# Performance work log

Hardware: AMD Instinct MI355X
Metric: run time of the kernel (lower is better)

## Reference

```python
import jax, jax.numpy as jnp
import numpy as np

# per-class illumination constants (19 Cityscapes classes), pre-divided by 255
_NIGHT = jnp.asarray(np.array([76.5113984140019, 76.23163212875781, 60.90662084364415, 69.06930071129905, 69.63671393061327, 73.11413822794262, 140.7827781957324, 116.29554873008291, 46.23329954488532, 57.839322341112386, 32.61465346757989, 57.4385179294615, 62.234896087294814, 90.90285758569436, 91.99610158117673, 91.82209397173472, 94.06478985576457, 74.6924145472464, 69.15034088822232], dtype=np.float32) / 255.0)
_CITY = jnp.asarray(np.array([86.46051320057052, 79.37014543897092, 95.30679177391578, 71.11888521745776, 75.57026559270716, 77.90493757655786, 74.77466800282637, 88.27701037425895, 57.685269557270146, 72.71472387765841, 229.9589238353863, 66.9194012998903, 60.42471796718752, 76.8407421534007, 74.98657626719087, 73.56771430328095, 123.92515568872523, 68.93476495876828, 76.0970460111028], dtype=np.float32) / 255.0)

LOSS_WEIGHT = 1.0
GAMMA = 0.4


def setup_inputs() -> dict:
    key = jax.random.key(0)
    k1, k2, k3 = jax.random.split(key, 3)
    B, H, W = 8, 512, 1024
    reflectance = jax.random.uniform(k1, (B, 3, H, W), dtype=jnp.float32)
    org_img = jax.random.uniform(k2, (B, 3, H, W), dtype=jnp.float32)
    seg_label = jax.random.randint(k3, (B, 1, H, W), 0, 19, dtype=jnp.int64)
    return {"reflectance": reflectance, "org_img": org_img, "seg_label": seg_label}


def reference(reflectance, org_img, seg_label):
    # illumination = channel-wise max: [B,1,H,W]
    illum = jnp.max(org_img, axis=1, keepdims=True)
    # the 19-way masked subtract loop is a per-pixel table gather
    illum = illum - _NIGHT[seg_label]
    # min-max normalize over the whole tensor
    imin, imax = illum.min(), illum.max()
    illum = (illum - imin) / (imax - imin)
    # gamma correction (faithful to gamma(): divide by max, pow, re-scale)
    gmax = illum.max()
    illum = jnp.power(illum / gmax, GAMMA) * gmax
    # 19-way masked add loop == gather of cityscape table
    illum = jnp.clip(illum + _CITY[seg_label], 0.0, 1.0)
    bright = reflectance * illum  # broadcast [B,3,H,W] * [B,1,H,W]
    mean = jnp.mean(bright, axis=(0, 2, 3))  # [3] per-channel means
    r, g, b = mean[0], mean[1], mean[2]
    loss = LOSS_WEIGHT * ((r - g) ** 2 + (r - b) ** 2 + (g - b) ** 2)
    return loss
```

## Files before the change

### kernel.cpp

```cpp
#include <hip/hip_runtime.h>

#define HW_C   524288
#define NPIX   4194304
#define NG     (NPIX / 4)
#define GRID   1024
#define BLK    256
#define SLICE  (GRID * BLK)

__device__ __forceinline__ float fast_pow04(float x) {
    return __builtin_amdgcn_exp2f(0.4f * __builtin_amdgcn_logf(x));
}

__constant__ float c_night[19] = {
    (float)(76.5113984140019/255.0),  (float)(76.23163212875781/255.0),
    (float)(60.90662084364415/255.0), (float)(69.06930071129905/255.0),
    (float)(69.63671393061327/255.0), (float)(73.11413822794262/255.0),
    (float)(140.7827781957324/255.0), (float)(116.29554873008291/255.0),
    (float)(46.23329954488532/255.0), (float)(57.839322341112386/255.0),
    (float)(32.61465346757989/255.0), (float)(57.4385179294615/255.0),
    (float)(62.234896087294814/255.0),(float)(90.90285758569436/255.0),
    (float)(91.99610158117673/255.0), (float)(91.82209397173472/255.0),
    (float)(94.06478985576457/255.0), (float)(74.6924145472464/255.0),
    (float)(69.15034088822232/255.0)
};
__constant__ float c_city[19] = {
    (float)(86.46051320057052/255.0), (float)(79.37014543897092/255.0),
    (float)(95.30679177391578/255.0), (float)(71.11888521745776/255.0),
    (float)(75.57026559270716/255.0), (float)(77.90493757655786/255.0),
    (float)(74.77466800282637/255.0), (float)(88.27701037425895/255.0),
    (float)(57.685269557270146/255.0),(float)(72.71472387765841/255.0),
    (float)(229.9589238353863/255.0), (float)(66.9194012998903/255.0),
    (float)(60.42471796718752/255.0), (float)(76.8407421534007/255.0),
    (float)(74.98657626719087/255.0), (float)(73.56771430328095/255.0),
    (float)(123.92515568872523/255.0),(float)(68.93476495876828/255.0),
    (float)(76.0970460111028/255.0)
};

template<bool STORE>
__global__ __launch_bounds__(BLK, 4) void k_pass1(const float* __restrict__ org,
                                                  const int* __restrict__ seg,
                                                  float* __restrict__ illum,
                                                  uchar4* __restrict__ seg8,
                                                  float2* __restrict__ bmm)
{
    const int lane = threadIdx.x & 63;
    const float night_reg = c_night[lane < 19 ? lane : 0];
    const int t = blockIdx.x * BLK + threadIdx.x;

    float4 R[4], G[4], Bc[4];
    int4   S[4];
    int    P[4];

    #pragma unroll
    for (int k = 0; k < 4; ++k) {
        const int p = (t + k * SLICE) << 2;
        P[k] = p;
        const size_t base = (size_t)(p >> 19) * (3 * HW_C) + (p & (HW_C - 1));
        R[k]  = *(const float4*)(org + base);
        G[k]  = *(const float4*)(org + base + HW_C);
        Bc[k] = *(const float4*)(org + base + 2 * HW_C);
        S[k]  = *(const int4*)(seg + p);
    }

    float lmin = 1e30f, lmax = -1e30f;
    #pragma unroll
    for (int k = 0; k < 4; ++k) {
        float4 il;
        il.x = fmaxf(fmaxf(R[k].x, G[k].x), Bc[k].x) - __shfl(night_reg, S[k].x);
        il.y = fmaxf(fmaxf(R[k].y, G[k].y), Bc[k].y) - __shfl(night_reg, S[k].y);
        il.z = fmaxf(fmaxf(R[k].z, G[k].z), Bc[k].z) - __shfl(night_reg, S[k].z);
        il.w = fmaxf(fmaxf(R[k].w, G[k].w), Bc[k].w) - __shfl(night_reg, S[k].w);
        if (STORE) {
            *(float4*)(illum + P[k]) = il;
            seg8[P[k] >> 2] = make_uchar4((unsigned char)S[k].x, (unsigned char)S[k].y,
                                          (unsigned char)S[k].z, (unsigned char)S[k].w);
        }
        lmin = fminf(lmin, fminf(fminf(il.x, il.y), fminf(il.z, il.w)));
        lmax = fmaxf(lmax, fmaxf(fmaxf(il.x, il.y), fmaxf(il.z, il.w)));
    }

    #pragma unroll
    for (int m = 1; m < 64; m <<= 1) {
        lmin = fminf(lmin, __shfl_xor(lmin, m));
        lmax = fmaxf(lmax, __shfl_xor(lmax, m));
    }
    __shared__ float smin[BLK / 64], smax[BLK / 64];
    const int wave = threadIdx.x >> 6;
    if ((threadIdx.x & 63) == 0) { smin[wave] = lmin; smax[wave] = lmax; }
    __syncthreads();
    if (threadIdx.x == 0) {
        float m = smin[0], M = smax[0];
        #pragma unroll
        for (int w = 1; w < BLK / 64; ++w) { m = fminf(m, smin[w]); M = fmaxf(M, smax[w]); }
        bmm[blockIdx.x] = make_float2(m, M);
    }
}

template<bool STORE>
__global__ __launch_bounds__(BLK, 4) void k_pass2(const float* __restrict__ refl,
                                                  const float* __restrict__ org,
                                                  const int* __restrict__ seg,
                                                  const float* __restrict__ illum,
                                                  const uchar4* __restrict__ seg8,
                                                  const float2* __restrict__ bmm,
                                                  double* __restrict__ partial)
{
    const int lane = threadIdx.x & 63;
    const float city_reg  = c_city[lane < 19 ? lane : 0];
    const float night_reg = c_night[lane < 19 ? lane : 0];
    const int t = blockIdx.x * BLK + threadIdx.x;

    float2 mm[16];
    #pragma unroll
    for (int k = 0; k < 16; ++k) mm[k] = bmm[lane + k * 64];

    int P[4];
    size_t baseA[4];
    #pragma unroll
    for (int k = 0; k < 4; ++k) {
        const int p = (t + k * SLICE) << 2;
        P[k] = p;
        baseA[k] = (size_t)(p >> 19) * (3 * HW_C) + (p & (HW_C - 1));
    }

    float4 il[4]; uchar4 q[4];
    float4 oR[4], oG[4], oB[4]; int4 sv[4];
    if (STORE) {
        #pragma unroll
        for (int k = 0; k < 4; ++k) {
            il[k] = *(const float4*)(illum + P[k]);
            q[k]  = seg8[P[k] >> 2];
        }
    } else {
        #pragma unroll
        for (int k = 0; k < 4; ++k) {
            oR[k] = *(const float4*)(org + baseA[k]);
            oG[k] = *(const float4*)(org + baseA[k] + HW_C);
            oB[k] = *(const float4*)(org + baseA[k] + 2 * HW_C);
            sv[k] = *(const int4*)(seg + P[k]);
        }
    }
    float4 rr[4], gg[4], bb[4];
    #pragma unroll
    for (int k = 0; k < 4; ++k) {
        rr[k] = *(const float4*)(refl + baseA[k]);
        gg[k] = *(const float4*)(refl + baseA[k] + HW_C);
        bb[k] = *(const float4*)(refl + baseA[k] + 2 * HW_C);
    }

    float lmin = mm[0].x, lmax = mm[0].y;
    #pragma unroll
    for (int k = 1; k < 16; ++k) { lmin = fminf(lmin, mm[k].x); lmax = fmaxf(lmax, mm[k].y); }
    #pragma unroll
    for (int m = 1; m < 64; m <<= 1) {
        lmin = fminf(lmin, __shfl_xor(lmin, m));
        lmax = fmaxf(lmax, __shfl_xor(lmax, m));
    }
    const float imin = lmin;
    const float inv  = 1.0f / (lmax - lmin);

    float sr = 0.f, sg = 0.f, sb = 0.f;
    #pragma unroll
    for (int k = 0; k < 4; ++k) {
        float c0, c1, c2, c3;
        if (STORE) {
            c0 = __shfl(city_reg, (int)q[k].x); c1 = __shfl(city_reg, (int)q[k].y);
            c2 = __shfl(city_reg, (int)q[k].z); c3 = __shfl(city_reg, (int)q[k].w);
        } else {
            il[k].x = fmaxf(fmaxf(oR[k].x, oG[k].x), oB[k].x) - __shfl(night_reg, sv[k].x);
            il[k].y = fmaxf(fmaxf(oR[k].y, oG[k].y), oB[k].y) - __shfl(night_reg, sv[k].y);
            il[k].z = fmaxf(fmaxf(oR[k].z, oG[k].z), oB[k].z) - __shfl(night_reg, sv[k].z);
            il[k].w = fmaxf(fmaxf(oR[k].w, oG[k].w), oB[k].w) - __shfl(night_reg, sv[k].w);
            c0 = __shfl(city_reg, sv[k].x); c1 = __shfl(city_reg, sv[k].y);
            c2 = __shfl(city_reg, sv[k].z); c3 = __shfl(city_reg, sv[k].w);
        }
        float x, z;
        x = (il[k].x - imin) * inv; z = fminf(fmaxf(fast_pow04(x) + c0, 0.f), 1.f);
        sr += rr[k].x * z; sg += gg[k].x * z; sb += bb[k].x * z;
        x = (il[k].y - imin) * inv; z = fminf(fmaxf(fast_pow04(x) + c1, 0.f), 1.f);
        sr += rr[k].y * z; sg += gg[k].y * z; sb += bb[k].y * z;
        x = (il[k].z - imin) * inv; z = fminf(fmaxf(fast_pow04(x) + c2, 0.f), 1.f);
        sr += rr[k].z * z; sg += gg[k].z * z; sb += bb[k].z * z;
        x = (il[k].w - imin) * inv; z = fminf(fmaxf(fast_pow04(x) + c3, 0.f), 1.f);
        sr += rr[k].w * z; sg += gg[k].w * z; sb += bb[k].w * z;
    }

    double vr = sr, vg = sg, vb = sb;
    for (int off = 32; off > 0; off >>= 1) {
        vr += __shfl_down(vr, off);
        vg += __shfl_down(vg, off);
        vb += __shfl_down(vb, off);
    }
    __shared__ double sh[3][BLK / 64];
    const int wave = threadIdx.x >> 6;
    if ((threadIdx.x & 63) == 0) { sh[0][wave] = vr; sh[1][wave] = vg; sh[2][wave] = vb; }
    __syncthreads();
    if (threadIdx.x == 0) {
        double tr = 0, tg = 0, tb = 0;
        #pragma unroll
        for (int w = 0; w < BLK / 64; ++w) { tr += sh[0][w]; tg += sh[1][w]; tb += sh[2][w]; }
        partial[3 * blockIdx.x + 0] = tr;
        partial[3 * blockIdx.x + 1] = tg;
        partial[3 * blockIdx.x + 2] = tb;
    }
}

__global__ __launch_bounds__(BLK) void k_final(const double* __restrict__ partial,
                                               float* __restrict__ out)
{
    double sr = 0, sg = 0, sb = 0;
    for (int i = threadIdx.x; i < GRID; i += BLK) {
        sr += partial[3 * i + 0];
        sg += partial[3 * i + 1];
        sb += partial[3 * i + 2];
    }
    for (int off = 32; off > 0; off >>= 1) {
        sr += __shfl_down(sr, off);
        sg += __shfl_down(sg, off);
        sb += __shfl_down(sb, off);
    }
    __shared__ double sh[3][BLK / 64];
    const int wave = threadIdx.x >> 6;
    if ((threadIdx.x & 63) == 0) { sh[0][wave] = sr; sh[1][wave] = sg; sh[2][wave] = sb; }
    __syncthreads();
    if (threadIdx.x == 0) {
        double tr = 0, tg = 0, tb = 0;
        #pragma unroll
        for (int w = 0; w < BLK / 64; ++w) { tr += sh[0][w]; tg += sh[1][w]; tb += sh[2][w]; }
        const double n = (double)NPIX;
        const double r = tr / n, g = tg / n, b = tb / n;
        out[0] = (float)((r - g) * (r - g) + (r - b) * (r - b) + (g - b) * (g - b));
    }
}

extern "C" void kernel_launch(void* const* d_in, const int* in_sizes, int n_in,
                              void* d_out, int out_size, void* d_ws, size_t ws_size,
                              hipStream_t stream) {
    const float* refl = (const float*)d_in[0];
    const float* org  = (const float*)d_in[1];
    const int*   seg  = (const int*)d_in[2];
    float* out = (float*)d_out;

    unsigned char* wsb = (unsigned char*)d_ws;
    float2*  bmm     = (float2*)(wsb + 4096);
    double*  partial = (double*)(wsb + 24576);
    float*   illum   = (float*)(wsb + 131072);
    uchar4*  seg8    = (uchar4*)(wsb + 131072 + sizeof(float) * (size_t)NPIX);
    const size_t needed = 131072 + 5ull * (size_t)NPIX;
    const bool store = (ws_size >= needed);

    if (store) {
        k_pass1<true ><<<GRID, BLK, 0, stream>>>(org, seg, illum, seg8, bmm);
        k_pass2<true ><<<GRID, BLK, 0, stream>>>(refl, org, seg, illum, seg8, bmm, partial);
    } else {
        k_pass1<false><<<GRID, BLK, 0, stream>>>(org, seg, illum, seg8, bmm);
        k_pass2<false><<<GRID, BLK, 0, stream>>>(refl, org, seg, illum, seg8, bmm, partial);
    }
    k_final<<<1, BLK, 0, stream>>>(partial, out);
}
```

Measured before the change: 138.0 us.

## Recompute illumination in second pass instead of materializing it to workspace

Removes the path that wrote per-pixel illumination and packed labels to workspace in the first pass and read them back in the second. The second pass now always re-reads org_img and seg_label and recomputes channel max minus the night table. This relies on those inputs still being resident in the large last-level cache from the first pass, and saves roughly 20 MB of writes. It also reads the block min/max array as float4, and moves the reflectance loads into the accumulation loop to lower register pressure. The trade-off is more raw read traffic if the re-reads miss the cache.

```diff
diff --git a/kernel.cpp b/kernel.cpp
--- a/kernel.cpp
+++ b/kernel.cpp
@@ -36,11 +36,8 @@
     (float)(76.0970460111028/255.0)
 };
 
-template<bool STORE>
 __global__ __launch_bounds__(BLK, 4) void k_pass1(const float* __restrict__ org,
                                                   const int* __restrict__ seg,
-                                                  float* __restrict__ illum,
-                                                  uchar4* __restrict__ seg8,
                                                   float2* __restrict__ bmm)
 {
     const int lane = threadIdx.x & 63;
@@ -49,12 +46,10 @@
 
     float4 R[4], G[4], Bc[4];
     int4   S[4];
-    int    P[4];
 
     #pragma unroll
     for (int k = 0; k < 4; ++k) {
         const int p = (t + k * SLICE) << 2;
-        P[k] = p;
         const size_t base = (size_t)(p >> 19) * (3 * HW_C) + (p & (HW_C - 1));
         R[k]  = *(const float4*)(org + base);
         G[k]  = *(const float4*)(org + base + HW_C);
@@ -70,11 +65,6 @@
         il.y = fmaxf(fmaxf(R[k].y, G[k].y), Bc[k].y) - __shfl(night_reg, S[k].y);
         il.z = fmaxf(fmaxf(R[k].z, G[k].z), Bc[k].z) - __shfl(night_reg, S[k].z);
         il.w = fmaxf(fmaxf(R[k].w, G[k].w), Bc[k].w) - __shfl(night_reg, S[k].w);
-        if (STORE) {
-            *(float4*)(illum + P[k]) = il;
-            seg8[P[k] >> 2] = make_uchar4((unsigned char)S[k].x, (unsigned char)S[k].y,
-                                          (unsigned char)S[k].z, (unsigned char)S[k].w);
-        }
         lmin = fminf(lmin, fminf(fminf(il.x, il.y), fminf(il.z, il.w)));
         lmax = fmaxf(lmax, fmaxf(fmaxf(il.x, il.y), fmaxf(il.z, il.w)));
     }
@@ -96,12 +86,9 @@
     }
 }
 
-template<bool STORE>
 __global__ __launch_bounds__(BLK, 4) void k_pass2(const float* __restrict__ refl,
                                                   const float* __restrict__ org,
                                                   const int* __restrict__ seg,
-                                                  const float* __restrict__ illum,
-                                                  const uchar4* __restrict__ seg8,
                                                   const float2* __restrict__ bmm,
                                                   double* __restrict__ partial)
 {
@@ -110,9 +97,10 @@
     const float night_reg = c_night[lane < 19 ? lane : 0];
     const int t = blockIdx.x * BLK + threadIdx.x;
 
-    float2 mm[16];
-    #pragma unroll
-    for (int k = 0; k < 16; ++k) mm[k] = bmm[lane + k * 64];
+    const float4* bmm4 = (const float4*)bmm;
+    float4 mm[8];
+    #pragma unroll
+    for (int k = 0; k < 8; ++k) mm[k] = bmm4[lane + k * 64];
 
     int P[4];
     size_t baseA[4];
@@ -123,34 +111,21 @@
         baseA[k] = (size_t)(p >> 19) * (3 * HW_C) + (p & (HW_C - 1));
     }
 
-    float4 il[4]; uchar4 q[4];
     float4 oR[4], oG[4], oB[4]; int4 sv[4];
-    if (STORE) {
-        #pragma unroll
-        for (int k = 0; k < 4; ++k) {
-            il[k] = *(const float4*)(illum + P[k]);
-            q[k]  = seg8[P[k] >> 2];
-        }
-    } else {
-        #pragma unroll
-        for (int k = 0; k < 4; ++k) {
-            oR[k] = *(const float4*)(org + baseA[k]);
-            oG[k] = *(const float4*)(org + baseA[k] + HW_C);
-            oB[k] = *(const float4*)(org + baseA[k] + 2 * HW_C);
-            sv[k] = *(const int4*)(seg + P[k]);
-        }
-    }
-    float4 rr[4], gg[4], bb[4];
-    #pragma unroll
-    for (int k = 0; k < 4; ++k) {
-        rr[k] = *(const float4*)(refl + baseA[k]);
-        gg[k] = *(const float4*)(refl + baseA[k] + HW_C);
-        bb[k] = *(const float4*)(refl + baseA[k] + 2 * HW_C);
-    }
-
-    float lmin = mm[0].x, lmax = mm[0].y;
-    #pragma unroll
-    for (int k = 1; k < 16; ++k) { lmin = fminf(lmin, mm[k].x); lmax = fmaxf(lmax, mm[k].y); }
+    #pragma unroll
+    for (int k = 0; k < 4; ++k) {
+        oR[k] = *(const float4*)(org + baseA[k]);
+        oG[k] = *(const float4*)(org + baseA[k] + HW_C);
+        oB[k] = *(const float4*)(org + baseA[k] + 2 * HW_C);
+        sv[k] = *(const int4*)(seg + P[k]);
+    }
+
+    float lmin = fminf(mm[0].x, mm[0].z), lmax = fmaxf(mm[0].y, mm[0].w);
+    #pragma unroll
+    for (int k = 1; k < 8; ++k) {
+        lmin = fminf(lmin, fminf(mm[k].x, mm[k].z));
+        lmax = fmaxf(lmax, fmaxf(mm[k].y, mm[k].w));
+    }
     #pragma unroll
     for (int m = 1; m < 64; m <<= 1) {
         lmin = fminf(lmin, __shfl_xor(lmin, m));
@@ -159,30 +134,33 @@
     const float imin = lmin;
     const float inv  = 1.0f / (lmax - lmin);
 
+    float4 il[4];
+    float  c[4][4];
+    #pragma unroll
+    for (int k = 0; k < 4; ++k) {
+        il[k].x = fmaxf(fmaxf(oR[k].x, oG[k].x), oB[k].x) - __shfl(night_reg, sv[k].x);
+        il[k].y = fmaxf(fmaxf(oR[k].y, oG[k].y), oB[k].y) - __shfl(night_reg, sv[k].y);
+        il[k].z = fmaxf(fmaxf(oR[k].z, oG[k].z), oB[k].z) - __shfl(night_reg, sv[k].z);
+        il[k].w = fmaxf(fmaxf(oR[k].w, oG[k].w), oB[k].w) - __shfl(night_reg, sv[k].w);
+        c[k][0] = __shfl(city_reg, sv[k].x); c[k][1] = __shfl(city_reg, sv[k].y);
+        c[k][2] = __shfl(city_reg, sv[k].z); c[k][3] = __shfl(city_reg, sv[k].w);
+    }
+
     float sr = 0.f, sg = 0.f, sb = 0.f;
     #pragma unroll
     for (int k = 0; k < 4; ++k) {
-        float c0, c1, c2, c3;
-        if (STORE) {
-            c0 = __shfl(city_reg, (int)q[k].x); c1 = __shfl(city_reg, (int)q[k].y);
-            c2 = __shfl(city_reg, (int)q[k].z); c3 = __shfl(city_reg, (int)q[k].w);
-        } else {
-            il[k].x = fmaxf(fmaxf(oR[k].x, oG[k].x), oB[k].x) - __shfl(night_reg, sv[k].x);
-            il[k].y = fmaxf(fmaxf(oR[k].y, oG[k].y), oB[k].y) - __shfl(night_reg, sv[k].y);
-            il[k].z = fmaxf(fmaxf(oR[k].z, oG[k].z), oB[k].z) - __shfl(night_reg, sv[k].z);
-            il[k].w = fmaxf(fmaxf(oR[k].w, oG[k].w), oB[k].w) - __shfl(night_reg, sv[k].w);
-            c0 = __shfl(city_reg, sv[k].x); c1 = __shfl(city_reg, sv[k].y);
-            c2 = __shfl(city_reg, sv[k].z); c3 = __shfl(city_reg, sv[k].w);
-        }
+        const float4 rr = *(const float4*)(refl + baseA[k]);
+        const float4 gg = *(const float4*)(refl + baseA[k] + HW_C);
+        const float4 bb = *(const float4*)(refl + baseA[k] + 2 * HW_C);
         float x, z;
-        x = (il[k].x - imin) * inv; z = fminf(fmaxf(fast_pow04(x) + c0, 0.f), 1.f);
-        sr += rr[k].x * z; sg += gg[k].x * z; sb += bb[k].x * z;
-        x = (il[k].y - imin) * inv; z = fminf(fmaxf(fast_pow04(x) + c1, 0.f), 1.f);
-        sr += rr[k].y * z; sg += gg[k].y * z; sb += bb[k].y * z;
-        x = (il[k].z - imin) * inv; z = fminf(fmaxf(fast_pow04(x) + c2, 0.f), 1.f);
-        sr += rr[k].z * z; sg += gg[k].z * z; sb += bb[k].z * z;
-        x = (il[k].w - imin) * inv; z = fminf(fmaxf(fast_pow04(x) + c3, 0.f), 1.f);
-        sr += rr[k].w * z; sg += gg[k].w * z; sb += bb[k].w * z;
+        x = (il[k].x - imin) * inv; z = fminf(fmaxf(fast_pow04(x) + c[k][0], 0.f), 1.f);
+        sr += rr.x * z; sg += gg.x * z; sb += bb.x * z;
+        x = (il[k].y - imin) * inv; z = fminf(fmaxf(fast_pow04(x) + c[k][1], 0.f), 1.f);
+        sr += rr.y * z; sg += gg.y * z; sb += bb.y * z;
+        x = (il[k].z - imin) * inv; z = fminf(fmaxf(fast_pow04(x) + c[k][2], 0.f), 1.f);
+        sr += rr.z * z; sg += gg.z * z; sb += bb.z * z;
+        x = (il[k].w - imin) * inv; z = fminf(fmaxf(fast_pow04(x) + c[k][3], 0.f), 1.f);
+        sr += rr.w * z; sg += gg.w * z; sb += bb.w * z;
     }
 
     double vr = sr, vg = sg, vb = sb;
@@ -242,19 +220,10 @@
     float* out = (float*)d_out;
 
     unsigned char* wsb = (unsigned char*)d_ws;
-    float2*  bmm     = (float2*)(wsb + 4096);
-    double*  partial = (double*)(wsb + 24576);
-    float*   illum   = (float*)(wsb + 131072);
-    uchar4*  seg8    = (uchar4*)(wsb + 131072 + sizeof(float) * (size_t)NPIX);
-    const size_t needed = 131072 + 5ull * (size_t)NPIX;
-    const bool store = (ws_size >= needed);
-
-    if (store) {
-        k_pass1<true ><<<GRID, BLK, 0, stream>>>(org, seg, illum, seg8, bmm);
-        k_pass2<true ><<<GRID, BLK, 0, stream>>>(refl, org, seg, illum, seg8, bmm, partial);
-    } else {
-        k_pass1<false><<<GRID, BLK, 0, stream>>>(org, seg, illum, seg8, bmm);
-        k_pass2<false><<<GRID, BLK, 0, stream>>>(refl, org, seg, illum, seg8, bmm, partial);
-    }
+    float2*  bmm     = (float2*)(wsb);
+    double*  partial = (double*)(wsb + 16384);
+
+    k_pass1<<<GRID, BLK, 0, stream>>>(org, seg, bmm);
+    k_pass2<<<GRID, BLK, 0, stream>>>(refl, org, seg, bmm, partial);
     k_final<<<1, BLK, 0, stream>>>(partial, out);
 }
```

Result: slower. 142.7 us (+3.4%).
